# Performance work log

Hardware: AMD Instinct MI355X
Metric: run time of the kernel (lower is better)

Reference implementation:

```python
import jax, jax.numpy as jnp
import numpy as np
import math

B, S, E, D = 8, 2048, 1024, 1024  # batch, seq, emb_dim, encoder_emb_dim
LN_EPS = 1e-5
CLAMP = 1.0e9

def setup_inputs() -> dict:
    key = jax.random.key(0)
    ks = jax.random.split(key, 6)
    s = 1.0 / math.sqrt(E)
    return {
        "x": jax.random.normal(ks[0], (B, S, E), dtype=jnp.float32),
        "ln_w": jnp.ones((E,), jnp.float32),
        "ln_b": jnp.zeros((E,), jnp.float32),
        "wq": jax.random.normal(ks[1], (E, D), jnp.float32) * s,
        "bq": jnp.zeros((D,), jnp.float32),
        "wk": jax.random.normal(ks[2], (E, D), jnp.float32) * s,
        "bk": jnp.zeros((D,), jnp.float32),
        "wv": jax.random.normal(ks[3], (E, D), jnp.float32) * s,
        "bv": jnp.zeros((D,), jnp.float32),
        "w0": jax.random.normal(ks[4], (D, E), jnp.float32) * (1.0 / math.sqrt(D)),
        "b0": jnp.zeros((E,), jnp.float32),
    }

def reference(x, ln_w, ln_b, wq, bq, wk, bk, wv, bv, w0, b0):
    # LayerNorm over last dim (torch default eps=1e-5)
    mu = jnp.mean(x, axis=-1, keepdims=True)
    var = jnp.mean(jnp.square(x - mu), axis=-1, keepdims=True)
    xn = (x - mu) * jax.lax.rsqrt(var + LN_EPS) * ln_w + ln_b

    q = xn @ wq + bq  # [B,S,D]
    k = xn @ wk + bk
    v = xn @ wv + bv

    scale = math.sqrt(D) + 1e-9
    scores = jnp.einsum("bsd,btd->bst", q, k) / scale
    scores = jnp.clip(scores, -CLAMP, CLAMP)

    # masking=True, self_attending=True: mask = tril(ones, diagonal=-1)
    # i.e. positions t < s get -inf; diagonal stays unmasked (no NaN rows).
    mask = jnp.tril(jnp.ones((S, S), dtype=bool), k=-1)
    scores = jnp.where(mask, -jnp.inf, scores)

    a = jax.nn.softmax(scores, axis=-1)
    h = jnp.einsum("bst,btd->bsd", a, v)
    return h @ w0 + b0
```

## Files before the change

### kernel.cpp

```cpp
#include <hip/hip_runtime.h>
#include <cmath>

using u16 = unsigned short;
using u32 = unsigned int;
using bf16x8 = __attribute__((ext_vector_type(8))) __bf16;
using f32x4  = __attribute__((ext_vector_type(4))) float;

__device__ inline u16 f2bf(float f) {
  u32 u = __float_as_uint(f);
  u32 r = (u + 0x7fffu + ((u >> 16) & 1u)) >> 16;
  return (u16)r;
}

__global__ __launch_bounds__(256) void ln_kernel(
    const float* __restrict__ x, const float* __restrict__ w,
    const float* __restrict__ b, u16* __restrict__ xn) {
  int row = blockIdx.x;
  const float4* xr = (const float4*)(x + (size_t)row * 1024);
  float4 v = xr[threadIdx.x];
  float s  = v.x + v.y + v.z + v.w;
  float ss = v.x * v.x + v.y * v.y + v.z * v.z + v.w * v.w;
  int lane = threadIdx.x & 63, wave = threadIdx.x >> 6;
#pragma unroll
  for (int o = 32; o >= 1; o >>= 1) {
    s  += __shfl_xor(s, o, 64);
    ss += __shfl_xor(ss, o, 64);
  }
  __shared__ float rs[4], rq[4];
  if (lane == 0) { rs[wave] = s; rq[wave] = ss; }
  __syncthreads();
  s  = rs[0] + rs[1] + rs[2] + rs[3];
  ss = rq[0] + rq[1] + rq[2] + rq[3];
  float mean = s * (1.0f / 1024.0f);
  float var  = ss * (1.0f / 1024.0f) - mean * mean;
  float rstd = rsqrtf(var + 1e-5f);
  int c = threadIdx.x * 4;
  ushort4 ov;
  ov.x = f2bf((v.x - mean) * rstd * w[c + 0] + b[c + 0]);
  ov.y = f2bf((v.y - mean) * rstd * w[c + 1] + b[c + 1]);
  ov.z = f2bf((v.z - mean) * rstd * w[c + 2] + b[c + 2]);
  ov.w = f2bf((v.w - mean) * rstd * w[c + 3] + b[c + 3]);
  ((ushort4*)(xn + (size_t)row * 1024))[threadIdx.x] = ov;
}

__global__ __launch_bounds__(256) void transpose_w4(
    const float* __restrict__ wq, const float* __restrict__ wk,
    const float* __restrict__ wv, const float* __restrict__ w0,
    u16* __restrict__ wqkvt, u16* __restrict__ w0t) {
  int z = blockIdx.z;
  const float* in = (z == 0) ? wq : (z == 1) ? wk : (z == 2) ? wv : w0;
  u16* out = (z < 3) ? (wqkvt + (size_t)z * 1024 * 1024) : w0t;
  __shared__ float tile[32][33];
  int c0 = blockIdx.x * 32, r0 = blockIdx.y * 32;
  int tx = threadIdx.x, ty = threadIdx.y;
#pragma unroll
  for (int i = 0; i < 32; i += 8)
    tile[ty + i][tx] = in[(size_t)(r0 + ty + i) * 1024 + c0 + tx];
  __syncthreads();
#pragma unroll
  for (int i = 0; i < 32; i += 8)
    out[(size_t)(c0 + ty + i) * 1024 + r0 + tx] = f2bf(tile[tx][ty + i]);
}

__global__ void concat_bias(const float* __restrict__ bq, const float* __restrict__ bk,
                            const float* __restrict__ bv, float* __restrict__ o) {
  int i = blockIdx.x * 1024 + threadIdx.x;
  const float* src = (blockIdx.x == 0) ? bq : (blockIdx.x == 1) ? bk : bv;
  o[i] = src[threadIdx.x];
}

template <int OUTF32, int MODE>
__global__ __launch_bounds__(512, 2) void gemm256(
    const u16* __restrict__ A, const u16* __restrict__ B, void* __restrict__ Cv,
    const float* __restrict__ bias, int K, int lda, int ldb, int ldc,
    float scale, long long sA, long long sB, long long sC) {
  int gx = gridDim.x;
  int wg = blockIdx.y * gx + blockIdx.x;
  {
    int nwg = gx * gridDim.y;
    if ((nwg & 7) == 0) {
      int q = nwg >> 3;
      wg = (wg & 7) * q + (wg >> 3);
    }
  }
  const int ti = wg / gx, tj = wg % gx, bz = blockIdx.z;
  if (MODE == 1 && tj < ti) return;

  const u16* Ab = A + (size_t)bz * (size_t)sA;
  const u16* Bb = B + (size_t)bz * (size_t)sB;

  __shared__ u16 As[2][256 * 64];
  __shared__ u16 Bs[2][256 * 64];

  const int tid = threadIdx.x;
  const int wave = tid >> 6, lane = tid & 63;
  const int wr = wave >> 2, wc = wave & 3;
  const int fr = lane & 15;
  const int kb16 = (lane >> 4) * 16;
  const int swz = (fr & 7) << 4;
  const int cs0 = kb16 ^ swz;
  const int cs1 = (64 + kb16) ^ swz;
  const int aRowOff = (wr * 128 + fr) * 128;
  const int bRowOff = (wc * 64 + fr) * 128;

  size_t gAo[2][2], gBo[2][2];
  u32 ldsA[2][2], ldsB[2][2];
#pragma unroll
  for (int h = 0; h < 2; ++h) {
#pragma unroll
    for (int l = 0; l < 2; ++l) {
      int i = l * 512 + tid;
      int rih = i >> 3, ch8 = i & 7;
      int rA = (rih & 63) + ((rih >> 6) << 7) + h * 64;
      int cbA = (ch8 << 4) ^ ((rA & 7) << 4);
      gAo[h][l] = (size_t)rA * lda + (cbA >> 1);
      ldsA[h][l] = (u32)(rA * 8 + ch8) * 16;
      int rB = (rih & 31) + ((rih >> 5) << 6) + h * 32;
      int cbB = (ch8 << 4) ^ ((rB & 7) << 4);
      gBo[h][l] = (size_t)rB * ldb + (cbB >> 1);
      ldsB[h][l] = (u32)(rB * 8 + ch8) * 16;
    }
  }
  const size_t aBase = (size_t)(ti * 256) * lda;
  const size_t bBase = (size_t)(tj * 256) * ldb;

  const int k0 = (MODE == 2) ? ti * 256 : 0;
  const int niter = (K - k0) / 128;

  f32x4 acc[8][4] = {};
  bf16x8 aF[4][2], bF[4][2];

#define GLL(gaddr, laddr)                                        \
  __builtin_amdgcn_global_load_lds(                              \
      (const __attribute__((address_space(1))) void*)(gaddr),    \
      (__attribute__((address_space(3))) void*)(laddr), 16, 0, 0)

#define STAGE_A(buf, h, t)                                                     \
  do {                                                                         \
    const size_t _kt = aBase + (size_t)(k0 + (t) * 64);                        \
    GLL(Ab + _kt + gAo[h][0], (char*)&As[buf][0] + ldsA[h][0]);                \
    GLL(Ab + _kt + gAo[h][1], (char*)&As[buf][0] + ldsA[h][1]);                \
  } while (0)
#define STAGE_B(buf, h, t)                                                     \
  do {                                                                         \
    const size_t _kt = bBase + (size_t)(k0 + (t) * 64);                        \
    GLL(Bb + _kt + gBo[h][0], (char*)&Bs[buf][0] + ldsB[h][0]);                \
    GLL(Bb + _kt + gBo[h][1], (char*)&Bs[buf][0] + ldsB[h][1]);                \
  } while (0)

#define DS_A(buf, qm)                                                \
  do {                                                               \
    const char* _pa = (const char*)&As[buf][0] + aRowOff + (qm)*8192;\
    _Pragma("unroll") for (int mm = 0; mm < 4; ++mm) {               \
      aF[mm][0] = *(const bf16x8*)(_pa + mm * 2048 + cs0);           \
      aF[mm][1] = *(const bf16x8*)(_pa + mm * 2048 + cs1);           \
    }                                                                \
  } while (0)
#define DS_B(buf, nh)                                                \
  do {                                                               \
    const char* _pb = (const char*)&Bs[buf][0] + bRowOff;            \
    _Pragma("unroll") for (int nn = 0; nn < 2; ++nn) {               \
      bF[(nh)*2 + nn][0] = *(const bf16x8*)(_pb + ((nh)*2 + nn) * 2048 + cs0); \
      bF[(nh)*2 + nn][1] = *(const bf16x8*)(_pb + ((nh)*2 + nn) * 2048 + cs1); \
    }                                                                \
  } while (0)

#define MMA(qm, nh)                                                          \
  do {                                                                       \
    _Pragma("unroll") for (int mm = 0; mm < 4; ++mm)                         \
    _Pragma("unroll") for (int nn = 0; nn < 2; ++nn) {                       \
      f32x4 _c = acc[(qm)*4 + mm][(nh)*2 + nn];                              \
      _c = __builtin_amdgcn_mfma_f32_16x16x32_bf16(aF[mm][0], bF[(nh)*2+nn][0], _c, 0, 0, 0); \
      _c = __builtin_amdgcn_mfma_f32_16x16x32_bf16(aF[mm][1], bF[(nh)*2+nn][1], _c, 0, 0, 0); \
      acc[(qm)*4 + mm][(nh)*2 + nn] = _c;                                    \
    }                                                                        \
  } while (0)

#define BAR __builtin_amdgcn_s_barrier()
#define LGKM0 asm volatile("s_waitcnt lgkmcnt(0)" ::: "memory")
#define VM6 asm volatile("s_waitcnt vmcnt(6)" ::: "memory")
#define VM0 asm volatile("s_waitcnt vmcnt(0)" ::: "memory")
#define PRIO1 __builtin_amdgcn_s_setprio(1)
#define PRIO0 __builtin_amdgcn_s_setprio(0)

  STAGE_B(0, 0, 0); STAGE_B(0, 1, 0); STAGE_A(0, 0, 0); STAGE_A(0, 1, 0);
  STAGE_B(1, 0, 1); STAGE_B(1, 1, 1); STAGE_A(1, 0, 1);
  VM6; BAR;

  for (int it = 0; it < niter; ++it) {
    const bool last = (it == niter - 1);
    const int t1g = 2 * it + 1, t2g = 2 * it + 2, t3g = 2 * it + 3;

    DS_A(0, 0); DS_B(0, 0);
    STAGE_A(1, 1, t1g);
    BAR; LGKM0; PRIO1; MMA(0, 0); PRIO0; BAR;
    DS_B(0, 1);
    if (!last) STAGE_B(0, 0, t2g);
    BAR; LGKM0; PRIO1; MMA(0, 1); PRIO0; BAR;
    DS_A(0, 1);
    if (!last) STAGE_B(0, 1, t2g);
    BAR; LGKM0; PRIO1; MMA(1, 0); PRIO0; BAR;
    if (!last) STAGE_A(0, 0, t2g);
    BAR; PRIO1; MMA(1, 1); PRIO0;
    if (last) { VM0; } else { VM6; }
    BAR;
    DS_A(1, 0); DS_B(1, 0);
    if (!last) STAGE_A(0, 1, t2g);
    BAR; LGKM0; PRIO1; MMA(0, 0); PRIO0; BAR;
    DS_B(1, 1);
    if (!last) STAGE_B(1, 0, t3g);
    BAR; LGKM0; PRIO1; MMA(0, 1); PRIO0; BAR;
    DS_A(1, 1);
    if (!last) STAGE_B(1, 1, t3g);
    BAR; LGKM0; PRIO1; MMA(1, 0); PRIO0; BAR;
    if (!last) STAGE_A(1, 0, t3g);
    BAR; PRIO1; MMA(1, 1); PRIO0;
    if (!last) VM6;
    BAR;
  }

  const int orow0 = ti * 256 + wr * 128 + ((lane >> 4) << 2);
  const int ocol0 = tj * 256 + wc * 64 + fr;
#pragma unroll
  for (int m = 0; m < 8; ++m) {
#pragma unroll
    for (int n = 0; n < 4; ++n) {
      const int col = ocol0 + n * 16;
      const float bv = bias ? bias[col] : 0.0f;
#pragma unroll
      for (int j = 0; j < 4; ++j) {
        const int row = orow0 + m * 16 + j;
        const float v = acc[m][n][j] * scale + bv;
        const size_t idx = (size_t)bz * (size_t)sC + (size_t)row * ldc + col;
        if (OUTF32) ((float*)Cv)[idx] = v;
        else        ((u16*)Cv)[idx]   = f2bf(v);
      }
    }
  }
#undef GLL
#undef STAGE_A
#undef STAGE_B
#undef DS_A
#undef DS_B
#undef MMA
#undef BAR
#undef LGKM0
#undef VM6
#undef VM0
#undef PRIO1
#undef PRIO0
}

template <int BM, int EPI, int LDA, int LDB, int LDC, int KK, int K0CT>
__device__ __forceinline__ void gemm_body(
    const u16* __restrict__ Ab, const u16* __restrict__ Bb,
    void* __restrict__ Cp, const float* __restrict__ bias,
    int rk0, float scale, size_t cbase, int ti, int tj,
    u16* __restrict__ AsP, u16* __restrict__ BsP,
    float* __restrict__ sumP, int diag) {
  constexpr int WM = BM / 2;
  constexpr int MH = BM / 64;
  constexpr int FM = 2 * MH;
  constexpr int HR = BM / 4;
  constexpr int LA = BM / 128;

  const int k0 = (K0CT >= 0) ? K0CT : rk0;

  const int tid = threadIdx.x;
  const int wave = tid >> 6, lane = tid & 63;
  const int wr = wave >> 2, wc = wave & 3;
  const int fr = lane & 15;
  const int kb16 = (lane >> 4) * 16;
  const int swz = (fr & 7) << 4;
  const int cs0 = kb16 ^ swz;
  const int cs1 = (64 + kb16) ^ swz;
  const int aRowOff = (wr * WM + fr) * 128;
  const int bRowOff = (wc * 64 + fr) * 128;

  __shared__ float invLds[(EPI == 2) ? BM : 1];
  if constexpr (EPI == 2) {
    if (tid < BM) {
      int s = ti * BM + tid;
      float a = 0.f;
      for (int q2 = s >> 8; q2 < 8; ++q2) a += sumP[q2 * 2048 + s];
      invLds[tid] = 1.0f / a;
    }
  }

  size_t gAo[2][LA], gBo[2][2];
  u32 ldsA[2][LA], ldsB[2][2];
#pragma unroll
  for (int h = 0; h < 2; ++h) {
#pragma unroll
    for (int l = 0; l < LA; ++l) {
      int i = l * 512 + tid;
      int rih = i >> 3, ch8 = i & 7;
      int rA = (rih % HR) + (rih / HR) * WM + h * HR;
      int cbA = (ch8 << 4) ^ ((rA & 7) << 4);
      gAo[h][l] = (size_t)rA * LDA + (cbA >> 1);
      ldsA[h][l] = (u32)(rA * 8 + ch8) * 16;
    }
#pragma unroll
    for (int l = 0; l < 2; ++l) {
      int i = l * 512 + tid;
      int rih = i >> 3, ch8 = i & 7;
      int rB = (rih & 31) + ((rih >> 5) << 6) + h * 32;
      int cbB = (ch8 << 4) ^ ((rB & 7) << 4);
      gBo[h][l] = (size_t)rB * LDB + (cbB >> 1);
      ldsB[h][l] = (u32)(rB * 8 + ch8) * 16;
    }
  }
  const size_t aBase = (size_t)(ti * BM) * LDA;
  const size_t bBase = (size_t)(tj * 256) * LDB;
  const int niter = (KK - k0) / 128;

  f32x4 acc[FM][4] = {};
  bf16x8 aF[MH][2], bF[4][2];

#define GLL(gaddr, laddr)                                        \
  __builtin_amdgcn_global_load_lds(                              \
      (const __attribute__((address_space(1))) void*)(gaddr),    \
      (__attribute__((address_space(3))) void*)(laddr), 16, 0, 0)

#define STAGE_A(buf, h, t)                                                   \
  do {                                                                       \
    const size_t _kt = aBase + (size_t)(k0 + (t) * 64);                      \
    _Pragma("unroll") for (int _l = 0; _l < LA; ++_l)                        \
        GLL(Ab + _kt + gAo[h][_l],                                           \
            (char*)(AsP + (buf) * (BM * 64)) + ldsA[h][_l]);                 \
  } while (0)
#define STAGE_B(buf, h, t)                                                   \
  do {                                                                       \
    const size_t _kt = bBase + (size_t)(k0 + (t) * 64);                      \
    _Pragma("unroll") for (int _l = 0; _l < 2; ++_l)                         \
        GLL(Bb + _kt + gBo[h][_l],                                           \
            (char*)(BsP + (buf) * (256 * 64)) + ldsB[h][_l]);                \
  } while (0)

#define DS_A(buf, qm)                                                        \
  do {                                                                       \
    const char* _pa =                                                        \
        (const char*)(AsP + (buf) * (BM * 64)) + aRowOff + (qm) * (MH * 2048); \
    _Pragma("unroll") for (int mm = 0; mm < MH; ++mm) {                      \
      aF[mm][0] = *(const bf16x8*)(_pa + mm * 2048 + cs0);                   \
      aF[mm][1] = *(const bf16x8*)(_pa + mm * 2048 + cs1);                   \
    }                                                                        \
  } while (0)
#define DS_B(buf, nh)                                                        \
  do {                                                                       \
    const char* _pb = (const char*)(BsP + (buf) * (256 * 64)) + bRowOff;     \
    _Pragma("unroll") for (int nn = 0; nn < 2; ++nn) {                       \
      bF[(nh)*2 + nn][0] = *(const bf16x8*)(_pb + ((nh)*2 + nn) * 2048 + cs0); \
      bF[(nh)*2 + nn][1] = *(const bf16x8*)(_pb + ((nh)*2 + nn) * 2048 + cs1); \
    }                                                                        \
  } while (0)

#define MMA(qm, nh)                                                          \
  do {                                                                       \
    _Pragma("unroll") for (int mm = 0; mm < MH; ++mm)                        \
    _Pragma("unroll") for (int nn = 0; nn < 2; ++nn) {                       \
      f32x4 _c = acc[(qm)*MH + mm][(nh)*2 + nn];                             \
      _c = __builtin_amdgcn_mfma_f32_16x16x32_bf16(aF[mm][0], bF[(nh)*2+nn][0], _c, 0, 0, 0); \
      _c = __builtin_amdgcn_mfma_f32_16x16x32_bf16(aF[mm][1], bF[(nh)*2+nn][1], _c, 0, 0, 0); \
      acc[(qm)*MH + mm][(nh)*2 + nn] = _c;                                   \
    }                                                                        \
  } while (0)

#define BAR __builtin_amdgcn_s_barrier()
#define LGKM0 asm volatile("s_waitcnt lgkmcnt(0)" ::: "memory")
#define VMN                                                                  \
  do {                                                                       \
    if constexpr (BM == 256)                                                 \
      asm volatile("s_waitcnt vmcnt(6)" ::: "memory");                       \
    else                                                                     \
      asm volatile("s_waitcnt vmcnt(5)" ::: "memory");                       \
  } while (0)
#define VM0 asm volatile("s_waitcnt vmcnt(0)" ::: "memory")
#define PRIO1 __builtin_amdgcn_s_setprio(1)
#define PRIO0 __builtin_amdgcn_s_setprio(0)

  STAGE_B(0, 0, 0); STAGE_B(0, 1, 0); STAGE_A(0, 0, 0); STAGE_A(0, 1, 0);
  STAGE_B(1, 0, 1); STAGE_B(1, 1, 1); STAGE_A(1, 0, 1);
  VMN; BAR;

#pragma unroll 1
  for (int it = 0; it < niter; ++it) {
    const bool last = (it == niter - 1);
    const int t1g = 2 * it + 1, t2g = 2 * it + 2, t3g = 2 * it + 3;

    DS_A(0, 0); DS_B(0, 0);
    STAGE_A(1, 1, t1g);
    BAR; LGKM0; PRIO1; MMA(0, 0); PRIO0; BAR;
    DS_B(0, 1);
    if (!last) STAGE_B(0, 0, t2g);
    BAR; LGKM0; PRIO1; MMA(0, 1); PRIO0; BAR;
    DS_A(0, 1);
    if (!last) STAGE_B(0, 1, t2g);
    BAR; LGKM0; PRIO1; MMA(1, 0); PRIO0; BAR;
    if (!last) STAGE_A(0, 0, t2g);
    BAR; PRIO1; MMA(1, 1); PRIO0;
    if (last) { VM0; } else { VMN; }
    BAR;
    DS_A(1, 0); DS_B(1, 0);
    if (!last) STAGE_A(0, 1, t2g);
    BAR; LGKM0; PRIO1; MMA(0, 0); PRIO0; BAR;
    DS_B(1, 1);
    if (!last) STAGE_B(1, 0, t3g);
    BAR; LGKM0; PRIO1; MMA(0, 1); PRIO0; BAR;
    DS_A(1, 1);
    if (!last) STAGE_B(1, 1, t3g);
    BAR; LGKM0; PRIO1; MMA(1, 0); PRIO0; BAR;
    if (!last) STAGE_A(1, 0, t3g);
    BAR; PRIO1; MMA(1, 1); PRIO0;
    if (!last) VMN;
    BAR;
  }

  const int orowL = wr * WM + ((lane >> 4) << 2);
  const int orow0 = ti * BM + orowL;
  const int ocol0 = tj * 256 + wc * 64 + fr;

  if constexpr (EPI == 1) {
    float* slds = (float*)AsP;
#pragma unroll
    for (int m = 0; m < FM; ++m) {
#pragma unroll
      for (int j = 0; j < 4; ++j) {
        const int rl = orowL + m * 16 + j;
        const int row = ti * BM + rl;
        float rsum = 0.f;
#pragma unroll
        for (int n = 0; n < 4; ++n) {
          const int cl = wc * 64 + fr + n * 16;
          float v = acc[m][n][j] * scale;
          v = fminf(fmaxf(v, -1.0e9f), 1.0e9f);
          v = fminf(v, 60.0f);
          float e = __expf(v - 5.0f);
          if (diag && cl < rl) e = 0.f;
          rsum += e;
          ((u16*)Cp)[cbase + (size_t)row * LDC + ocol0 + n * 16] = f2bf(e);
        }
        rsum += __shfl_xor(rsum, 1, 64);
        rsum += __shfl_xor(rsum, 2, 64);
        rsum += __shfl_xor(rsum, 4, 64);
        rsum += __shfl_xor(rsum, 8, 64);
        if (fr == 0) slds[rl * 4 + wc] = rsum;
      }
    }
    __syncthreads();
    if (tid < BM) {
      float t = slds[tid * 4 + 0] + slds[tid * 4 + 1] +
                slds[tid * 4 + 2] + slds[tid * 4 + 3];
      sumP[ti * BM + tid] = t;
    }
  } else {
#pragma unroll
    for (int m = 0; m < FM; ++m) {
#pragma unroll
      for (int j = 0; j < 4; ++j) {
        const int row = orow0 + m * 16 + j;
        float mul = (EPI == 2) ? invLds[orowL + m * 16 + j] : 1.0f;
#pragma unroll
        for (int n = 0; n < 4; ++n) {
          const int col = ocol0 + n * 16;
          const float bv = bias ? bias[col] : 0.0f;
          const size_t idx = cbase + (size_t)row * LDC + col;
          if constexpr (EPI == 2) {
            ((float*)Cp)[idx] = acc[m][n][j] * mul + bv;
          } else {
            ((u16*)Cp)[idx] = f2bf(acc[m][n][j] + bv);
          }
        }
      }
    }
  }
#undef GLL
#undef STAGE_A
#undef STAGE_B
#undef DS_A
#undef DS_B
#undef MMA
#undef BAR
#undef LGKM0
#undef VMN
#undef VM0
#undef PRIO1
#undef PRIO0
}

__global__ __launch_bounds__(512, 2) void gemm_qkwt(
    const u16* __restrict__ QKVp, const u16* __restrict__ w0t,
    u16* __restrict__ Wt, u16* __restrict__ sc, float* __restrict__ sumP,
    int qkBlocks, int b0, int nb, float qk_scale) {
  __shared__ u16 As[2][256 * 64];
  __shared__ u16 Bs[2][256 * 64];
  const long long sQKV = 2048LL * 3072, sWt = 1024LL * 2048, sS = 2048LL * 2048;
  int x = blockIdx.x;
  if (x < qkBlocks) {
    int bzl = x % nb, t36 = x / nb;
    int bz = b0 + bzl;
    int tj = 0, accm = 0;
    while (t36 >= accm + tj + 1) { accm += tj + 1; ++tj; }
    int tq = t36 - accm;
    const u16* Ab = QKVp + (size_t)bz * sQKV;
    gemm_body<256, 1, 3072, 3072, 2048, 1024, 0>(
        Ab, Ab + 1024, sc, nullptr, 0, qk_scale, (size_t)bzl * sS,
        tq, tj, &As[0][0], &Bs[0][0],
        sumP + ((size_t)bz * 8 + tj) * 2048, tq == tj);
  } else {
    int x2 = x - qkBlocks;
    int bz = x2 & 7;
    int o = x2 >> 3;
    int ti = o & 7, tj = o >> 3;
    gemm_body<128, 0, 1024, 3072, 2048, 1024, 0>(
        w0t, QKVp + (size_t)bz * sQKV + 2048, Wt, nullptr, 0, 1.0f,
        (size_t)bz * sWt, ti, tj, &As[0][0], &Bs[0][0], nullptr, 0);
  }
}

__global__ __launch_bounds__(512, 2) void gemm_pv(
    const u16* __restrict__ sc, const u16* __restrict__ Wt,
    float* __restrict__ out, const float* __restrict__ b0v,
    float* __restrict__ sumP, int nb, int bA) {
  __shared__ u16 As[2][128 * 64];
  __shared__ u16 Bs[2][256 * 64];
  const long long sP = 2048LL * 2048, sWt = 1024LL * 2048, sH = 2048LL * 1024;
  int x = blockIdx.x;
  int bzl = x % nb;
  int rem = x / nb;
  int ti = rem >> 2, tj = rem & 3;
  int bz = bA + bzl;
  gemm_body<128, 2, 2048, 2048, 1024, 2048, -1>(
      sc + (size_t)bzl * sP, Wt + (size_t)bz * sWt, out, b0v, ti * 128, 1.0f,
      (size_t)bz * sH, ti, tj, &As[0][0], &Bs[0][0],
      sumP + (size_t)bz * 8 * 2048, 0);
}

extern "C" void kernel_launch(void* const* d_in, const int* in_sizes, int n_in,
                              void* d_out, int out_size, void* d_ws, size_t ws_size,
                              hipStream_t stream) {
  (void)in_sizes; (void)n_in; (void)out_size;
  const float* x   = (const float*)d_in[0];
  const float* lnw = (const float*)d_in[1];
  const float* lnb = (const float*)d_in[2];
  const float* wq  = (const float*)d_in[3];
  const float* bq  = (const float*)d_in[4];
  const float* wk  = (const float*)d_in[5];
  const float* bk  = (const float*)d_in[6];
  const float* wv  = (const float*)d_in[7];
  const float* bv  = (const float*)d_in[8];
  const float* w0  = (const float*)d_in[9];
  const float* b0  = (const float*)d_in[10];
  float* out = (float*)d_out;

  const size_t ROWS = 16384;
  char* ws = (char*)d_ws;
  size_t off = 0;
  auto alloc = [&](size_t bytes) -> void* {
    void* p = ws + off;
    off += (bytes + 255) & ~(size_t)255;
    return p;
  };
  u16*   xn    = (u16*)alloc(ROWS * 1024 * 2);
  u16*   wqkvt = (u16*)alloc((size_t)3072 * 1024 * 2);
  u16*   w0t   = (u16*)alloc((size_t)1024 * 1024 * 2);
  float* bqkv  = (float*)alloc(3072 * 4);
  float* sumP  = (float*)alloc((size_t)8 * 8 * 2048 * 4);
  u16*   QKV   = (u16*)alloc(ROWS * 3072 * 2);
  u16*   Wt    = (u16*)alloc(ROWS * 1024 * 2);

  const size_t CHUNK1 = (size_t)2048 * 2048 * 2;
  size_t avail = (ws_size > off) ? ws_size - off : 0;
  int NBCH = (int)(avail / CHUNK1);
  if (NBCH > 8) NBCH = 8;
  if (NBCH < 1) NBCH = 1;
  u16* sc = (u16*)(ws + off);

  ln_kernel<<<dim3(16384), dim3(256), 0, stream>>>(x, lnw, lnb, xn);
  transpose_w4<<<dim3(32, 32, 4), dim3(32, 8), 0, stream>>>(
      wq, wk, wv, w0, wqkvt, w0t);
  concat_bias<<<dim3(3), dim3(1024), 0, stream>>>(bq, bk, bv, bqkv);

  gemm256<0, 0><<<dim3(12, 64, 1), dim3(512), 0, stream>>>(
      xn, wqkvt, QKV, bqkv, 1024, 1024, 1024, 3072, 1.0f, 0, 0, 0);

  float qk_scale = (float)(1.0 / (std::sqrt(1024.0) + 1e-9));

  for (int bA = 0; bA < 8; bA += NBCH) {
    int nb = 8 - bA;
    if (nb > NBCH) nb = NBCH;
    int qkB = nb * 36;
    int wtB = (bA == 0) ? 512 : 0;
    gemm_qkwt<<<dim3(qkB + wtB), dim3(512), 0, stream>>>(
        QKV, w0t, Wt, sc, sumP, qkB, bA, nb, qk_scale);
    gemm_pv<<<dim3(64 * nb), dim3(512), 0, stream>>>(
        sc, Wt, out, b0, sumP, nb, bA);
  }
}
```

Baseline: 304.7 us.

## Fold Q/K/V weights into precomputed Wq·Wkᵀ and Wv·W0 products

Scores are now computed as xn·(Wq Wkᵀ)·xnᵀ, with the bias terms split into per-row and per-column vectors, so Q and K are never materialized. V·W0 is folded into a precomputed Wv·W0 product applied to xn. This replaces the 3072-wide QKV projection with a 1024-wide xn·G GEMM plus small weight-weight GEMMs, and fuses the layer norm, weight casts and bias dot products into one prep kernel. The QK tile shape changes from 256 to 128 rows with diagonal-offset masking. Precomputing the weight products in bf16 adds a rounding step, which may change accuracy.

New measurement: 320.4 us. 5.2% more time.

```diff
diff --git a/kernel.cpp b/kernel.cpp
--- a/kernel.cpp
+++ b/kernel.cpp
@@ -11,62 +11,99 @@
   u32 r = (u + 0x7fffu + ((u >> 16) & 1u)) >> 16;
   return (u16)r;
 }
-
-__global__ __launch_bounds__(256) void ln_kernel(
-    const float* __restrict__ x, const float* __restrict__ w,
-    const float* __restrict__ b, u16* __restrict__ xn) {
-  int row = blockIdx.x;
-  const float4* xr = (const float4*)(x + (size_t)row * 1024);
-  float4 v = xr[threadIdx.x];
-  float s  = v.x + v.y + v.z + v.w;
-  float ss = v.x * v.x + v.y * v.y + v.z * v.z + v.w * v.w;
-  int lane = threadIdx.x & 63, wave = threadIdx.x >> 6;
-#pragma unroll
-  for (int o = 32; o >= 1; o >>= 1) {
-    s  += __shfl_xor(s, o, 64);
-    ss += __shfl_xor(ss, o, 64);
-  }
-  __shared__ float rs[4], rq[4];
-  if (lane == 0) { rs[wave] = s; rq[wave] = ss; }
-  __syncthreads();
-  s  = rs[0] + rs[1] + rs[2] + rs[3];
-  ss = rq[0] + rq[1] + rq[2] + rq[3];
-  float mean = s * (1.0f / 1024.0f);
-  float var  = ss * (1.0f / 1024.0f) - mean * mean;
-  float rstd = rsqrtf(var + 1e-5f);
-  int c = threadIdx.x * 4;
-  ushort4 ov;
-  ov.x = f2bf((v.x - mean) * rstd * w[c + 0] + b[c + 0]);
-  ov.y = f2bf((v.y - mean) * rstd * w[c + 1] + b[c + 1]);
-  ov.z = f2bf((v.z - mean) * rstd * w[c + 2] + b[c + 2]);
-  ov.w = f2bf((v.w - mean) * rstd * w[c + 3] + b[c + 3]);
-  ((ushort4*)(xn + (size_t)row * 1024))[threadIdx.x] = ov;
-}
-
-__global__ __launch_bounds__(256) void transpose_w4(
-    const float* __restrict__ wq, const float* __restrict__ wk,
-    const float* __restrict__ wv, const float* __restrict__ w0,
-    u16* __restrict__ wqkvt, u16* __restrict__ w0t) {
-  int z = blockIdx.z;
-  const float* in = (z == 0) ? wq : (z == 1) ? wk : (z == 2) ? wv : w0;
-  u16* out = (z < 3) ? (wqkvt + (size_t)z * 1024 * 1024) : w0t;
-  __shared__ float tile[32][33];
-  int c0 = blockIdx.x * 32, r0 = blockIdx.y * 32;
-  int tx = threadIdx.x, ty = threadIdx.y;
-#pragma unroll
-  for (int i = 0; i < 32; i += 8)
-    tile[ty + i][tx] = in[(size_t)(r0 + ty + i) * 1024 + c0 + tx];
-  __syncthreads();
-#pragma unroll
-  for (int i = 0; i < 32; i += 8)
-    out[(size_t)(c0 + ty + i) * 1024 + r0 + tx] = f2bf(tile[tx][ty + i]);
-}
-
-__global__ void concat_bias(const float* __restrict__ bq, const float* __restrict__ bk,
-                            const float* __restrict__ bv, float* __restrict__ o) {
-  int i = blockIdx.x * 1024 + threadIdx.x;
-  const float* src = (blockIdx.x == 0) ? bq : (blockIdx.x == 1) ? bk : bv;
-  o[i] = src[threadIdx.x];
+__device__ inline float bf2f(u16 v) { return __uint_as_float(((u32)v) << 16); }
+
+__global__ __launch_bounds__(256) void prep1(
+    const float* __restrict__ x, const float* __restrict__ lnw,
+    const float* __restrict__ lnb, const float* __restrict__ wq,
+    const float* __restrict__ wk, const float* __restrict__ wv,
+    const float* __restrict__ w0, const float* __restrict__ bq,
+    const float* __restrict__ bk, const float* __restrict__ bv,
+    u16* __restrict__ xn, u16* __restrict__ w0t, u16* __restrict__ wqb,
+    u16* __restrict__ wkb, u16* __restrict__ wvb, float* __restrict__ uvec,
+    float* __restrict__ vvec, float* __restrict__ wb, float* __restrict__ sb) {
+  int b = blockIdx.x;
+  int tid = threadIdx.x;
+  __shared__ float red[4];
+  __shared__ float red2[4];
+  int lane = tid & 63, wave = tid >> 6;
+  if (b < 16384) {
+    const float4* xr = (const float4*)(x + (size_t)b * 1024);
+    float4 v = xr[tid];
+    float s  = v.x + v.y + v.z + v.w;
+    float ss = v.x * v.x + v.y * v.y + v.z * v.z + v.w * v.w;
+#pragma unroll
+    for (int o = 32; o >= 1; o >>= 1) {
+      s  += __shfl_xor(s, o, 64);
+      ss += __shfl_xor(ss, o, 64);
+    }
+    if (lane == 0) { red[wave] = s; red2[wave] = ss; }
+    __syncthreads();
+    s  = red[0] + red[1] + red[2] + red[3];
+    ss = red2[0] + red2[1] + red2[2] + red2[3];
+    float mean = s * (1.0f / 1024.0f);
+    float var  = ss * (1.0f / 1024.0f) - mean * mean;
+    float rstd = rsqrtf(var + 1e-5f);
+    int c = tid * 4;
+    ushort4 ov;
+    ov.x = f2bf((v.x - mean) * rstd * lnw[c + 0] + lnb[c + 0]);
+    ov.y = f2bf((v.y - mean) * rstd * lnw[c + 1] + lnb[c + 1]);
+    ov.z = f2bf((v.z - mean) * rstd * lnw[c + 2] + lnb[c + 2]);
+    ov.w = f2bf((v.w - mean) * rstd * lnw[c + 3] + lnb[c + 3]);
+    ((ushort4*)(xn + (size_t)b * 1024))[tid] = ov;
+  } else if (b < 17408) {
+    int b2 = b - 16384;
+    int c0 = (b2 & 31) * 32, r0 = (b2 >> 5) * 32;
+    int tx = tid & 31, ty = tid >> 5;
+    __shared__ float tile[32][33];
+#pragma unroll
+    for (int i = 0; i < 32; i += 8)
+      tile[ty + i][tx] = w0[(size_t)(r0 + ty + i) * 1024 + c0 + tx];
+    __syncthreads();
+#pragma unroll
+    for (int i = 0; i < 32; i += 8)
+      w0t[(size_t)(c0 + ty + i) * 1024 + r0 + tx] = f2bf(tile[tx][ty + i]);
+  } else if (b < 18944) {
+    int b3 = b - 17408;
+    int mat = b3 / 512, blk = b3 % 512;
+    const float* src = (mat == 0) ? wq : (mat == 1) ? wk : wv;
+    u16* dst = (mat == 0) ? wqb : (mat == 1) ? wkb : wvb;
+    size_t base = (size_t)blk * 2048 + (size_t)tid * 8;
+#pragma unroll
+    for (int i = 0; i < 8; ++i) dst[base + i] = f2bf(src[base + i]);
+  } else if (b < 22016) {
+    int b4 = b - 18944;
+    int which = b4 >> 10, idx = b4 & 1023;
+    float p = 0.f;
+    if (which == 0) {
+      const float* r = wq + (size_t)idx * 1024;
+      for (int e = tid * 4; e < (tid + 1) * 4; ++e) p += r[e] * bk[e];
+    } else if (which == 1) {
+      const float* r = wk + (size_t)idx * 1024;
+      for (int e = tid * 4; e < (tid + 1) * 4; ++e) p += r[e] * bq[e];
+    } else {
+      for (int d = tid * 4; d < (tid + 1) * 4; ++d)
+        p += bv[d] * w0[(size_t)d * 1024 + idx];
+    }
+#pragma unroll
+    for (int o = 32; o >= 1; o >>= 1) p += __shfl_xor(p, o, 64);
+    if (lane == 0) red[wave] = p;
+    __syncthreads();
+    if (tid == 0) {
+      float t = red[0] + red[1] + red[2] + red[3];
+      if (which == 0) uvec[idx] = t;
+      else if (which == 1) vvec[idx] = t;
+      else wb[idx] = t;
+    }
+  } else {
+    float p = 0.f;
+    for (int e = tid * 4; e < (tid + 1) * 4; ++e) p += bq[e] * bk[e];
+#pragma unroll
+    for (int o = 32; o >= 1; o >>= 1) p += __shfl_xor(p, o, 64);
+    if (lane == 0) red[wave] = p;
+    __syncthreads();
+    if (tid == 0) sb[0] = red[0] + red[1] + red[2] + red[3];
+  }
 }
 
 template <int OUTF32, int MODE>
@@ -255,9 +292,10 @@
 __device__ __forceinline__ void gemm_body(
     const u16* __restrict__ Ab, const u16* __restrict__ Bb,
     void* __restrict__ Cp, const float* __restrict__ bias,
-    int rk0, float scale, size_t cbase, int ti, int tj,
-    u16* __restrict__ AsP, u16* __restrict__ BsP,
-    float* __restrict__ sumP, int diag) {
+    const float* __restrict__ rbias, int rk0, float scale, size_t cbase,
+    int ti, int tj, u16* __restrict__ AsP, u16* __restrict__ BsP,
+    float* __restrict__ sumP, int dco,
+    const float* __restrict__ ruP, const float* __restrict__ rvP) {
   constexpr int WM = BM / 2;
   constexpr int MH = BM / 64;
   constexpr int FM = 2 * MH;
@@ -428,17 +466,19 @@
       for (int j = 0; j < 4; ++j) {
         const int rl = orowL + m * 16 + j;
         const int row = ti * BM + rl;
+        const float ru = ruP[row];
         float rsum = 0.f;
 #pragma unroll
         for (int n = 0; n < 4; ++n) {
           const int cl = wc * 64 + fr + n * 16;
-          float v = acc[m][n][j] * scale;
+          const int col = tj * 256 + cl;
+          float v = (acc[m][n][j] + ru + rvP[col]) * scale;
           v = fminf(fmaxf(v, -1.0e9f), 1.0e9f);
           v = fminf(v, 60.0f);
           float e = __expf(v - 5.0f);
-          if (diag && cl < rl) e = 0.f;
+          if (cl < rl + dco) e = 0.f;
           rsum += e;
-          ((u16*)Cp)[cbase + (size_t)row * LDC + ocol0 + n * 16] = f2bf(e);
+          ((u16*)Cp)[cbase + (size_t)row * LDC + col] = f2bf(e);
         }
         rsum += __shfl_xor(rsum, 1, 64);
         rsum += __shfl_xor(rsum, 2, 64);
@@ -460,6 +500,7 @@
       for (int j = 0; j < 4; ++j) {
         const int row = orow0 + m * 16 + j;
         float mul = (EPI == 2) ? invLds[orowL + m * 16 + j] : 1.0f;
+        float rb = (EPI == 0 && rbias) ? rbias[row] : 0.0f;
 #pragma unroll
         for (int n = 0; n < 4; ++n) {
           const int col = ocol0 + n * 16;
@@ -468,7 +509,7 @@
           if constexpr (EPI == 2) {
             ((float*)Cp)[idx] = acc[m][n][j] * mul + bv;
           } else {
-            ((u16*)Cp)[idx] = f2bf(acc[m][n][j] + bv);
+            ((u16*)Cp)[idx] = f2bf(acc[m][n][j] + bv + rb);
           }
         }
       }
@@ -488,34 +529,88 @@
 #undef PRIO0
 }
 
-__global__ __launch_bounds__(512, 2) void gemm_qkwt(
-    const u16* __restrict__ QKVp, const u16* __restrict__ w0t,
-    u16* __restrict__ Wt, u16* __restrict__ sc, float* __restrict__ sumP,
-    int qkBlocks, int b0, int nb, float qk_scale) {
-  __shared__ u16 As[2][256 * 64];
+__global__ __launch_bounds__(512, 2) void prep2(
+    const u16* __restrict__ wqb, const u16* __restrict__ wkb,
+    const u16* __restrict__ wvb, const u16* __restrict__ w0t,
+    const u16* __restrict__ xn, const float* __restrict__ uvec,
+    const float* __restrict__ vvec, const float* __restrict__ sb,
+    u16* __restrict__ Gt, u16* __restrict__ Uw,
+    float* __restrict__ ru, float* __restrict__ rv) {
+  __shared__ u16 As[2][128 * 64];
   __shared__ u16 Bs[2][256 * 64];
-  const long long sQKV = 2048LL * 3072, sWt = 1024LL * 2048, sS = 2048LL * 2048;
+  int b = blockIdx.x;
+  if (b < 32) {
+    int ti = b & 7, tj = b >> 3;
+    gemm_body<128, 0, 1024, 1024, 1024, 1024, 0>(
+        wkb, wqb, Gt, nullptr, nullptr, 0, 1.0f, 0, ti, tj,
+        &As[0][0], &Bs[0][0], nullptr, 0, nullptr, nullptr);
+  } else if (b < 64) {
+    int b2 = b - 32;
+    int ti = b2 & 7, tj = b2 >> 3;
+    gemm_body<128, 0, 1024, 1024, 1024, 1024, 0>(
+        w0t, wvb, Uw, nullptr, nullptr, 0, 1.0f, 0, ti, tj,
+        &As[0][0], &Bs[0][0], nullptr, 0, nullptr, nullptr);
+  } else {
+    int r = b - 64;
+    int tid = threadIdx.x;
+    const u16* row = xn + (size_t)r * 1024;
+    float pu = 0.f, pv = 0.f;
+    int c = tid * 2;
+    float x0 = bf2f(row[c]), x1 = bf2f(row[c + 1]);
+    pu = x0 * uvec[c] + x1 * uvec[c + 1];
+    pv = x0 * vvec[c] + x1 * vvec[c + 1];
+#pragma unroll
+    for (int o = 32; o >= 1; o >>= 1) {
+      pu += __shfl_xor(pu, o, 64);
+      pv += __shfl_xor(pv, o, 64);
+    }
+    __shared__ float rdu[8], rdv[8];
+    int lane = tid & 63, wave = tid >> 6;
+    if (lane == 0) { rdu[wave] = pu; rdv[wave] = pv; }
+    __syncthreads();
+    if (tid == 0) {
+      float su = 0.f, sv = 0.f;
+#pragma unroll
+      for (int w = 0; w < 8; ++w) { su += rdu[w]; sv += rdv[w]; }
+      ru[r] = su + sb[0];
+      rv[r] = sv;
+    }
+  }
+}
+
+__global__ __launch_bounds__(512, 2) void wt_kernel(
+    const u16* __restrict__ Uw, const u16* __restrict__ xn,
+    u16* __restrict__ Wt, const float* __restrict__ wb) {
+  __shared__ u16 As[2][128 * 64];
+  __shared__ u16 Bs[2][256 * 64];
   int x = blockIdx.x;
-  if (x < qkBlocks) {
-    int bzl = x % nb, t36 = x / nb;
-    int bz = b0 + bzl;
-    int tj = 0, accm = 0;
-    while (t36 >= accm + tj + 1) { accm += tj + 1; ++tj; }
-    int tq = t36 - accm;
-    const u16* Ab = QKVp + (size_t)bz * sQKV;
-    gemm_body<256, 1, 3072, 3072, 2048, 1024, 0>(
-        Ab, Ab + 1024, sc, nullptr, 0, qk_scale, (size_t)bzl * sS,
-        tq, tj, &As[0][0], &Bs[0][0],
-        sumP + ((size_t)bz * 8 + tj) * 2048, tq == tj);
-  } else {
-    int x2 = x - qkBlocks;
-    int bz = x2 & 7;
-    int o = x2 >> 3;
-    int ti = o & 7, tj = o >> 3;
-    gemm_body<128, 0, 1024, 3072, 2048, 1024, 0>(
-        w0t, QKVp + (size_t)bz * sQKV + 2048, Wt, nullptr, 0, 1.0f,
-        (size_t)bz * sWt, ti, tj, &As[0][0], &Bs[0][0], nullptr, 0);
-  }
+  int bz = x & 7, o = x >> 3;
+  int ti = o & 7, tj = o >> 3;
+  gemm_body<128, 0, 1024, 1024, 2048, 1024, 0>(
+      Uw, xn + (size_t)bz * 2048 * 1024, Wt, nullptr, wb, 0, 1.0f,
+      (size_t)bz * 1024 * 2048, ti, tj, &As[0][0], &Bs[0][0],
+      nullptr, 0, nullptr, nullptr);
+}
+
+__global__ __launch_bounds__(512, 2) void qk_kernel(
+    const u16* __restrict__ xnG, const u16* __restrict__ xn,
+    u16* __restrict__ sc, float* __restrict__ sumP,
+    const float* __restrict__ ru, const float* __restrict__ rv,
+    int b0, int nb, float qk_scale) {
+  __shared__ u16 As[2][128 * 64];
+  __shared__ u16 Bs[2][256 * 64];
+  int x = blockIdx.x;
+  int bzl = x % nb, t72 = x / nb;
+  int bz = b0 + bzl;
+  int tq = 0, rem = t72;
+  for (;;) { int L = 8 - (tq >> 1); if (rem < L) break; rem -= L; ++tq; }
+  int tj = (tq >> 1) + rem;
+  int dco = tq * 128 - tj * 256;
+  gemm_body<128, 1, 1024, 1024, 2048, 1024, 0>(
+      xnG + (size_t)bz * 2048 * 1024, xn + (size_t)bz * 2048 * 1024, sc,
+      nullptr, nullptr, 0, qk_scale, (size_t)bzl * 2048 * 2048, tq, tj,
+      &As[0][0], &Bs[0][0], sumP + ((size_t)bz * 8 + tj) * 2048, dco,
+      ru + (size_t)bz * 2048, rv + (size_t)bz * 2048);
 }
 
 __global__ __launch_bounds__(512, 2) void gemm_pv(
@@ -524,16 +619,16 @@
     float* __restrict__ sumP, int nb, int bA) {
   __shared__ u16 As[2][128 * 64];
   __shared__ u16 Bs[2][256 * 64];
-  const long long sP = 2048LL * 2048, sWt = 1024LL * 2048, sH = 2048LL * 1024;
   int x = blockIdx.x;
   int bzl = x % nb;
   int rem = x / nb;
   int ti = rem >> 2, tj = rem & 3;
   int bz = bA + bzl;
   gemm_body<128, 2, 2048, 2048, 1024, 2048, -1>(
-      sc + (size_t)bzl * sP, Wt + (size_t)bz * sWt, out, b0v, ti * 128, 1.0f,
-      (size_t)bz * sH, ti, tj, &As[0][0], &Bs[0][0],
-      sumP + (size_t)bz * 8 * 2048, 0);
+      sc + (size_t)bzl * 2048 * 2048, Wt + (size_t)bz * 1024 * 2048, out, b0v,
+      nullptr, ti * 128, 1.0f, (size_t)bz * 2048 * 1024, ti, tj,
+      &As[0][0], &Bs[0][0], sumP + (size_t)bz * 8 * 2048, 0,
+      nullptr, nullptr);
 }
 
 extern "C" void kernel_launch(void* const* d_in, const int* in_sizes, int n_in,
@@ -561,13 +656,22 @@
     off += (bytes + 255) & ~(size_t)255;
     return p;
   };
-  u16*   xn    = (u16*)alloc(ROWS * 1024 * 2);
-  u16*   wqkvt = (u16*)alloc((size_t)3072 * 1024 * 2);
-  u16*   w0t   = (u16*)alloc((size_t)1024 * 1024 * 2);
-  float* bqkv  = (float*)alloc(3072 * 4);
-  float* sumP  = (float*)alloc((size_t)8 * 8 * 2048 * 4);
-  u16*   QKV   = (u16*)alloc(ROWS * 3072 * 2);
-  u16*   Wt    = (u16*)alloc(ROWS * 1024 * 2);
+  u16*   xn   = (u16*)alloc(ROWS * 1024 * 2);
+  u16*   w0t  = (u16*)alloc((size_t)1024 * 1024 * 2);
+  u16*   wqb  = (u16*)alloc((size_t)1024 * 1024 * 2);
+  u16*   wkb  = (u16*)alloc((size_t)1024 * 1024 * 2);
+  u16*   wvb  = (u16*)alloc((size_t)1024 * 1024 * 2);
+  u16*   Gt   = (u16*)alloc((size_t)1024 * 1024 * 2);
+  u16*   Uw   = (u16*)alloc((size_t)1024 * 1024 * 2);
+  float* uvec = (float*)alloc(1024 * 4);
+  float* vvec = (float*)alloc(1024 * 4);
+  float* wb   = (float*)alloc(1024 * 4);
+  float* sb   = (float*)alloc(256);
+  float* ru   = (float*)alloc(ROWS * 4);
+  float* rv   = (float*)alloc(ROWS * 4);
+  float* sumP = (float*)alloc((size_t)8 * 8 * 2048 * 4);
+  u16*   xnG  = (u16*)alloc(ROWS * 1024 * 2);
+  u16*   Wt   = (u16*)alloc(ROWS * 1024 * 2);
 
   const size_t CHUNK1 = (size_t)2048 * 2048 * 2;
   size_t avail = (ws_size > off) ? ws_size - off : 0;
@@ -576,23 +680,22 @@
   if (NBCH < 1) NBCH = 1;
   u16* sc = (u16*)(ws + off);
 
-  ln_kernel<<<dim3(16384), dim3(256), 0, stream>>>(x, lnw, lnb, xn);
-  transpose_w4<<<dim3(32, 32, 4), dim3(32, 8), 0, stream>>>(
-      wq, wk, wv, w0, wqkvt, w0t);
-  concat_bias<<<dim3(3), dim3(1024), 0, stream>>>(bq, bk, bv, bqkv);
-
-  gemm256<0, 0><<<dim3(12, 64, 1), dim3(512), 0, stream>>>(
-      xn, wqkvt, QKV, bqkv, 1024, 1024, 1024, 3072, 1.0f, 0, 0, 0);
+  prep1<<<dim3(22017), dim3(256), 0, stream>>>(
+      x, lnw, lnb, wq, wk, wv, w0, bq, bk, bv,
+      xn, w0t, wqb, wkb, wvb, uvec, vvec, wb, sb);
+  prep2<<<dim3(64 + 16384), dim3(512), 0, stream>>>(
+      wqb, wkb, wvb, w0t, xn, uvec, vvec, sb, Gt, Uw, ru, rv);
+  gemm256<0, 0><<<dim3(4, 64, 1), dim3(512), 0, stream>>>(
+      xn, Gt, xnG, nullptr, 1024, 1024, 1024, 1024, 1.0f, 0, 0, 0);
+  wt_kernel<<<dim3(512), dim3(512), 0, stream>>>(Uw, xn, Wt, wb);
 
   float qk_scale = (float)(1.0 / (std::sqrt(1024.0) + 1e-9));
 
   for (int bA = 0; bA < 8; bA += NBCH) {
     int nb = 8 - bA;
     if (nb > NBCH) nb = NBCH;
-    int qkB = nb * 36;
-    int wtB = (bA == 0) ? 512 : 0;
-    gemm_qkwt<<<dim3(qkB + wtB), dim3(512), 0, stream>>>(
-        QKV, w0t, Wt, sc, sumP, qkB, bA, nb, qk_scale);
+    qk_kernel<<<dim3(nb * 72), dim3(512), 0, stream>>>(
+        xnG, xn, sc, sumP, ru, rv, bA, nb, qk_scale);
     gemm_pv<<<dim3(64 * nb), dim3(512), 0, stream>>>(
         sc, Wt, out, b0, sumP, nb, bA);
   }
```
